# Optimization experiments

Hardware: AMD Instinct MI355X
Metric: run time of the kernel (lower is better)

Reference implementation:

```python
import jax, jax.numpy as jnp
import numpy as np

N_NODES = 100000
N_EDGES = 3200000
IN_CH = 256
HIDDEN = 64
OUT_CH = 128


def setup_inputs() -> dict:
    key = jax.random.key(0)
    ks = jax.random.split(key, 6)
    x = jax.random.normal(ks[0], (N_NODES, IN_CH), dtype=jnp.float32)
    edge_index = jax.random.randint(ks[1], (2, N_EDGES), 0, N_NODES, dtype=jnp.int64)
    W1 = jax.random.normal(ks[2], (IN_CH, HIDDEN), dtype=jnp.float32) * (1.0 / np.sqrt(IN_CH))
    b1 = jnp.zeros((HIDDEN,), dtype=jnp.float32)
    W2 = jax.random.normal(ks[3], (HIDDEN, OUT_CH), dtype=jnp.float32) * (1.0 / np.sqrt(HIDDEN))
    b2 = jnp.zeros((OUT_CH,), dtype=jnp.float32)
    fcW = jax.random.normal(ks[4], (2, OUT_CH), dtype=jnp.float32) * (1.0 / np.sqrt(OUT_CH))
    fcb = jnp.zeros((2,), dtype=jnp.float32)
    return {"x": x, "edge_index": edge_index, "W1": W1, "b1": b1,
            "W2": W2, "b2": b2, "fcW": fcW, "fcb": fcb}


def _gcn_conv(x, edge_index, W, b):
    """PyG GCNConv: linear transform, add self-loops, symmetric D^-1/2 A D^-1/2 aggregation, bias."""
    N = x.shape[0]
    h = x @ W  # [N, F_out]
    loops = jnp.arange(N, dtype=edge_index.dtype)
    row = jnp.concatenate([edge_index[0], loops])  # source nodes
    col = jnp.concatenate([edge_index[1], loops])  # destination nodes
    deg = jax.ops.segment_sum(jnp.ones_like(col, dtype=h.dtype), col, num_segments=N)
    dinv = jnp.where(deg > 0, jax.lax.rsqrt(deg), 0.0)
    norm = dinv[row] * dinv[col]  # [E+N]
    out = jax.ops.segment_sum(h[row] * norm[:, None], col, num_segments=N)
    return out + b


def reference(x, edge_index, W1, b1, W2, b2, fcW, fcb):
    h = jax.nn.relu(_gcn_conv(x, edge_index, W1, b1))
    h = jax.nn.relu(_gcn_conv(h, edge_index, W2, b2))
    g = jnp.mean(h, axis=0)  # [OUT_CH]
    return g @ fcW.T + fcb   # [2]
```

## Files before the change

kernel.cpp:

```cpp
#include <hip/hip_runtime.h>

#define N_NODES 100000
#define N_EDGES 3200000
#define C_IN 256
#define C_H 64
#define C_OUT 128
#define NB 391
#define G2F 625
#define NTILES 6250
#define CH1 8192

typedef unsigned int u32;
typedef unsigned short u16;
typedef unsigned long long u64;
typedef __attribute__((ext_vector_type(8))) short bf16x8;
typedef __attribute__((ext_vector_type(4))) float f32x4;

__device__ __forceinline__ float bflo(u32 p) {
    union { u32 i; float f; } v; v.i = p << 16; return v.f;
}
__device__ __forceinline__ float bfhi(u32 p) {
    union { u32 i; float f; } v; v.i = p & 0xffff0000u; return v.f;
}
__device__ __forceinline__ float bf2f(u16 u) {
    union { u32 i; float f; } v; v.i = ((u32)u) << 16; return v.f;
}
__device__ __forceinline__ u16 f2bf(float f) {
    union { float f; u32 i; } v; v.f = f;
    u32 x = v.i;
    return (u16)((x + 0x7fffu + ((x >> 16) & 1u)) >> 16);
}

__global__ void k_detect(const void* __restrict__ x, const void* __restrict__ ei,
                         const void* __restrict__ b1, const void* __restrict__ b2,
                         const void* __restrict__ fcW, const void* __restrict__ fcb,
                         int* __restrict__ flags,
                         float* __restrict__ b1c, float* __restrict__ b2c,
                         float* __restrict__ fcWc, float* __restrict__ fcbc) {
    __shared__ int sf[2];
    int t = threadIdx.x;
    if (t < 64) {
        u32 w = ((const u32*)x)[t];
        u32 low = w & 0xffffu;
        int e = (int)((low >> 7) & 0xff);
        bool inw = (e > 96 && e < 160) || (low == 0);
        u64 m = __ballot(inw);
        if (t == 0) sf[0] = (__popcll(m) >= 60) ? 1 : 0;
    } else if (t < 128) {
        int i = t - 64;
        u32 w = ((const u32*)ei)[2 * i + 1];
        u64 m = __ballot(w == 0);
        if (i == 0) sf[1] = (m == ~0ull) ? 1 : 0;
    }
    __syncthreads();
    if (t == 0) { flags[0] = sf[0]; flags[1] = sf[1]; }
    int isbf = sf[0];
    if (isbf) {
        const u16* p1 = (const u16*)b1;  const u16* p2 = (const u16*)b2;
        const u16* pw = (const u16*)fcW; const u16* pb = (const u16*)fcb;
        for (int i = t; i < C_H; i += 256) b1c[i] = bf2f(p1[i]);
        for (int i = t; i < C_OUT; i += 256) b2c[i] = bf2f(p2[i]);
        for (int i = t; i < 2 * C_OUT; i += 256) fcWc[i] = bf2f(pw[i]);
        for (int i = t; i < 2; i += 256) fcbc[i] = bf2f(pb[i]);
    } else {
        const float* p1 = (const float*)b1;  const float* p2 = (const float*)b2;
        const float* pw = (const float*)fcW; const float* pb = (const float*)fcb;
        for (int i = t; i < C_H; i += 256) b1c[i] = p1[i];
        for (int i = t; i < C_OUT; i += 256) b2c[i] = p2[i];
        for (int i = t; i < 2 * C_OUT; i += 256) fcWc[i] = pw[i];
        for (int i = t; i < 2; i += 256) fcbc[i] = pb[i];
    }
}

__global__ __launch_bounds__(256) void k_prep(const void* __restrict__ W1,
                                              const void* __restrict__ W2,
                                              const int* __restrict__ flags,
                                              u16* __restrict__ W1m, u16* __restrict__ W2m,
                                              u32* __restrict__ bucket_cnt) {
    int b = blockIdx.x, t = threadIdx.x;
    int isbf = flags[0];
    int i = b * 256 + t;
    if (i < NB) bucket_cnt[i] = 0;
    if (i < C_IN * C_H) {
        const u16* w1b = (const u16*)W1; const float* w1f = (const float*)W1;
        int j = i & 7, lane = (i >> 3) & 63, nt = (i >> 9) & 3, k0 = i >> 11;
        int k = k0 * 32 + ((lane >> 4) & 3) * 8 + j;
        int n = nt * 16 + (lane & 15);
        W1m[i] = isbf ? w1b[k * C_H + n] : f2bf(w1f[k * C_H + n]);
    } else {
        int i2 = i - C_IN * C_H;
        const u16* w2b = (const u16*)W2; const float* w2f = (const float*)W2;
        int j = i2 & 7, lane = (i2 >> 3) & 63, nt = (i2 >> 9) & 7, k0 = (i2 >> 12) & 1;
        int k = k0 * 32 + ((lane >> 4) & 3) * 8 + j;
        int n = nt * 16 + (lane & 15);
        W2m[i2] = isbf ? w2b[k * C_OUT + n] : f2bf(w2f[k * C_OUT + n]);
    }
}

__global__ __launch_bounds__(256) void k_hist1(const int* __restrict__ ei,
                                               const int* __restrict__ flags,
                                               u32* __restrict__ bucket_cnt) {
    __shared__ u32 h[NB];
    int t = threadIdx.x;
    int is64 = flags[1];
    for (int i = t; i < NB; i += 256) h[i] = 0;
    __syncthreads();
    int e0 = blockIdx.x * CH1;
    int nv = min(CH1, N_EDGES - e0);
    for (int i = t; i < nv; i += 256) {
        int e = e0 + i;
        int d = is64 ? ei[2 * (N_EDGES + e)] : ei[N_EDGES + e];
        atomicAdd(&h[d >> 8], 1u);
    }
    __syncthreads();
    for (int i = t; i < NB; i += 256)
        if (h[i]) atomicAdd(&bucket_cnt[i], h[i]);
}

__global__ __launch_bounds__(512) void k_bscan(const u32* __restrict__ bucket_cnt,
                                               u32* __restrict__ bucket_base,
                                               u32* __restrict__ bucket_cursor,
                                               int* __restrict__ rowptr) {
    __shared__ u32 sm[512];
    int t = threadIdx.x;
    u32 v = (t < NB) ? bucket_cnt[t] : 0;
    sm[t] = v;
    __syncthreads();
    for (int off = 1; off < 512; off <<= 1) {
        u32 a = (t >= off) ? sm[t - off] : 0;
        __syncthreads();
        sm[t] += a;
        __syncthreads();
    }
    if (t < NB) {
        u32 excl = sm[t] - v;
        bucket_base[t] = excl;
        bucket_cursor[t] = excl;
    }
    if (t == 0) {
        bucket_base[NB] = N_EDGES;
        rowptr[N_NODES] = N_EDGES;
    }
}

__global__ __launch_bounds__(512) void k_scatter1(const int* __restrict__ ei,
                                                  const int* __restrict__ flags,
                                                  u32* __restrict__ bucket_cursor,
                                                  u32* __restrict__ ebuf) {
    __shared__ u32 cnt[NB];
    __shared__ u32 lcur[NB];
    __shared__ u32 gbase[NB];
    __shared__ u32 lofs[512];
    __shared__ u32 stp[CH1];
    __shared__ u16 stb[CH1];
    int t = threadIdx.x;
    int is64 = flags[1];
    int e0 = blockIdx.x * CH1;
    int nv = min(CH1, N_EDGES - e0);
    for (int i = t; i < NB; i += 512) { cnt[i] = 0; lcur[i] = 0; }
    __syncthreads();
    for (int i = t; i < nv; i += 512) {
        int e = e0 + i;
        int d = is64 ? ei[2 * (N_EDGES + e)] : ei[N_EDGES + e];
        atomicAdd(&cnt[d >> 8], 1u);
    }
    __syncthreads();
    u32 v = (t < NB) ? cnt[t] : 0;
    lofs[t] = v;
    __syncthreads();
    for (int off = 1; off < 512; off <<= 1) {
        u32 a = (t >= off) ? lofs[t - off] : 0;
        __syncthreads();
        lofs[t] += a;
        __syncthreads();
    }
    u32 excl = lofs[t] - v;
    __syncthreads();
    lofs[t] = excl;
    __syncthreads();
    for (int i = t; i < nv; i += 512) {
        int e = e0 + i;
        int d, s;
        if (is64) { d = ei[2 * (N_EDGES + e)]; s = ei[2 * e]; }
        else      { d = ei[N_EDGES + e];       s = ei[e]; }
        int b = d >> 8;
        u32 slot = lofs[b] + atomicAdd(&lcur[b], 1u);
        stp[slot] = ((u32)(d & 255) << 20) | (u32)s;
        stb[slot] = (u16)b;
    }
    __syncthreads();
    for (int b = t; b < NB; b += 512) {
        u32 c = cnt[b];
        gbase[b] = c ? atomicAdd(&bucket_cursor[b], c) : 0;
    }
    __syncthreads();
    for (int s = t; s < nv; s += 512) {
        int b = stb[s];
        ebuf[gbase[b] + (s - lofs[b])] = stp[s];
    }
}

__global__ __launch_bounds__(256) void k_scatter2(const u32* __restrict__ bucket_base,
                                                  const u32* __restrict__ ebuf,
                                                  int* __restrict__ rowptr,
                                                  float* __restrict__ dinv,
                                                  int* __restrict__ csr) {
    __shared__ int cnt[256];
    __shared__ int pfx[256];
    __shared__ int lcur[256];
    int b = blockIdx.x, t = threadIdx.x;
    int ebeg = (int)bucket_base[b], eend = (int)bucket_base[b + 1];
    cnt[t] = 0;
    lcur[t] = 0;
    __syncthreads();
    for (int i = ebeg + t; i < eend; i += 256)
        atomicAdd(&cnt[(ebuf[i] >> 20) & 255], 1);
    __syncthreads();
    int v = cnt[t];
    pfx[t] = v;
    __syncthreads();
    for (int off = 1; off < 256; off <<= 1) {
        int a = (t >= off) ? pfx[t - off] : 0;
        __syncthreads();
        pfx[t] += a;
        __syncthreads();
    }
    int node = (b << 8) + t;
    if (node < N_NODES) {
        rowptr[node] = ebeg + (pfx[t] - v);
        dinv[node] = rsqrtf((float)(v + 1));
    }
    __syncthreads();
    for (int i = ebeg + t; i < eend; i += 256) {
        u32 p = ebuf[i];
        int dl = (p >> 20) & 255;
        int pos = ebeg + (pfx[dl] - cnt[dl]) + atomicAdd(&lcur[dl], 1);
        csr[pos] = (int)(p & 0x1FFFFu);
    }
}

__global__ __launch_bounds__(256) void k_gemm1(const void* __restrict__ xv,
                                               const u16* __restrict__ W1m,
                                               const float* __restrict__ dinv,
                                               u16* __restrict__ g1,
                                               const int* __restrict__ flags) {
    __shared__ u16 wlds[C_IN * C_H];
    int t = threadIdx.x;
    int isbf = flags[0];
    {
        const uint4* src = (const uint4*)W1m;
        uint4* dst = (uint4*)wlds;
#pragma unroll
        for (int it = 0; it < 8; ++it) dst[t + it * 256] = src[t + it * 256];
    }
    __syncthreads();
    int w = t >> 6, lane = t & 63;
    int quad = lane >> 4, mrow = lane & 15;
    int m0 = blockIdx.x * 128 + w * 32;
    if (m0 >= N_NODES) return;

    bf16x8 a[2][8];
    if (isbf) {
        const u16* xb = (const u16*)xv;
#pragma unroll
        for (int mt = 0; mt < 2; ++mt)
#pragma unroll
            for (int k0 = 0; k0 < 8; ++k0)
                a[mt][k0] = *(const bf16x8*)(xb + (size_t)(m0 + mt * 16 + mrow) * C_IN + k0 * 32 + quad * 8);
    } else {
        const float* xf = (const float*)xv;
#pragma unroll
        for (int mt = 0; mt < 2; ++mt)
#pragma unroll
            for (int k0 = 0; k0 < 8; ++k0) {
                const float* p = xf + (size_t)(m0 + mt * 16 + mrow) * C_IN + k0 * 32 + quad * 8;
                float4 v0 = *(const float4*)p;
                float4 v1 = *(const float4*)(p + 4);
                bf16x8 r;
                r[0] = (short)f2bf(v0.x); r[1] = (short)f2bf(v0.y);
                r[2] = (short)f2bf(v0.z); r[3] = (short)f2bf(v0.w);
                r[4] = (short)f2bf(v1.x); r[5] = (short)f2bf(v1.y);
                r[6] = (short)f2bf(v1.z); r[7] = (short)f2bf(v1.w);
                a[mt][k0] = r;
            }
    }

    float dv0[4], dv1[4];
#pragma unroll
    for (int r = 0; r < 4; ++r) {
        dv0[r] = dinv[m0 + quad * 4 + r];
        dv1[r] = dinv[m0 + 16 + quad * 4 + r];
    }

#pragma unroll
    for (int nt = 0; nt < 4; ++nt) {
        bf16x8 b[8];
#pragma unroll
        for (int k0 = 0; k0 < 8; ++k0)
            b[k0] = *(const bf16x8*)&wlds[((k0 * 4 + nt) * 64 + lane) * 8];
        f32x4 acc0 = {0.f, 0.f, 0.f, 0.f};
        f32x4 acc1 = {0.f, 0.f, 0.f, 0.f};
#pragma unroll
        for (int k0 = 0; k0 < 8; ++k0) {
            acc0 = __builtin_amdgcn_mfma_f32_16x16x32_bf16(a[0][k0], b[k0], acc0, 0, 0, 0);
            acc1 = __builtin_amdgcn_mfma_f32_16x16x32_bf16(a[1][k0], b[k0], acc1, 0, 0, 0);
        }
        int ch = nt * 16 + mrow;
#pragma unroll
        for (int r = 0; r < 4; ++r) {
            g1[(size_t)(m0 + quad * 4 + r) * C_H + ch] = f2bf(acc0[r] * dv0[r]);
            g1[(size_t)(m0 + 16 + quad * 4 + r) * C_H + ch] = f2bf(acc1[r] * dv1[r]);
        }
    }
}

template <int MODE>
__global__ __launch_bounds__(256) void k_gatherT(const int* __restrict__ rowptr,
                                                 const int* __restrict__ csr_src,
                                                 const float* __restrict__ dinv,
                                                 const u16* __restrict__ g,
                                                 const float* __restrict__ bias,
                                                 void* __restrict__ outv) {
    int t = threadIdx.x;
    int w = t >> 6, lane = t & 63;
    int half = lane >> 5, j = lane & 31;
    int n = blockIdx.x * 8 + w * 2 + half;
    int beg = rowptr[n], end = rowptr[n + 1];
    float sA = 0.f, sB = 0.f;
    int e = beg;
    for (; e + 7 < end; e += 8) {
        int s[8]; u32 p[8];
#pragma unroll
        for (int q = 0; q < 8; ++q) s[q] = csr_src[e + q];
#pragma unroll
        for (int q = 0; q < 8; ++q) p[q] = *(const u32*)(g + s[q] * C_H + 2 * j);
#pragma unroll
        for (int q = 0; q < 8; ++q) {
            sA += bflo(p[q]);
            sB += bfhi(p[q]);
        }
    }
    for (; e + 3 < end; e += 4) {
        int s[4]; u32 p[4];
#pragma unroll
        for (int q = 0; q < 4; ++q) s[q] = csr_src[e + q];
#pragma unroll
        for (int q = 0; q < 4; ++q) p[q] = *(const u32*)(g + s[q] * C_H + 2 * j);
#pragma unroll
        for (int q = 0; q < 4; ++q) {
            sA += bflo(p[q]);
            sB += bfhi(p[q]);
        }
    }
    for (; e < end; ++e) {
        int s0 = csr_src[e];
        u32 p0 = *(const u32*)(g + s0 * C_H + 2 * j);
        sA += bflo(p0);
        sB += bfhi(p0);
    }
    float dn = dinv[n];
    u32 gn = *(const u32*)(g + n * C_H + 2 * j);
    float vA = dn * (sA + bflo(gn));
    float vB = dn * (sB + bfhi(gn));
    if (MODE == 0) {
        float aA = fmaxf(vA + bias[2 * j], 0.f);
        float aB = fmaxf(vB + bias[2 * j + 1], 0.f);
        u32 pk = (u32)f2bf(dn * aA) | ((u32)f2bf(dn * aB) << 16);
        ((u32*)outv)[n * 32 + j] = pk;
    } else {
        ((float2*)outv)[n * 32 + j] = make_float2(vA, vB);
    }
}

__global__ __launch_bounds__(256) void k_fused2(const float* __restrict__ agg,
                                                const u16* __restrict__ W2m,
                                                const float* __restrict__ b2c,
                                                float* __restrict__ partial) {
    __shared__ float psum[4 * 8 * 64];
    int t = threadIdx.x;
    int w = t >> 6, lane = t & 63;
    int quad = lane >> 4, m = lane & 15;

    bf16x8 b[2][8];
#pragma unroll
    for (int k0 = 0; k0 < 2; ++k0)
#pragma unroll
        for (int nt = 0; nt < 8; ++nt)
            b[k0][nt] = *(const bf16x8*)&W2m[((k0 * 8 + nt) * 64 + lane) * 8];

    float pacc[8] = {0.f, 0.f, 0.f, 0.f, 0.f, 0.f, 0.f, 0.f};
    float bias[8];
#pragma unroll
    for (int nt = 0; nt < 8; ++nt) bias[nt] = b2c[nt * 16 + m];

    for (int tile = blockIdx.x * 4 + w; tile < NTILES; tile += G2F * 4) {
        const float* arow = agg + (size_t)(tile * 16 + m) * C_H + quad * 8;
        bf16x8 a[2];
#pragma unroll
        for (int k0 = 0; k0 < 2; ++k0) {
            float4 v0 = *(const float4*)(arow + k0 * 32);
            float4 v1 = *(const float4*)(arow + k0 * 32 + 4);
            bf16x8 r;
            r[0] = (short)f2bf(v0.x); r[1] = (short)f2bf(v0.y);
            r[2] = (short)f2bf(v0.z); r[3] = (short)f2bf(v0.w);
            r[4] = (short)f2bf(v1.x); r[5] = (short)f2bf(v1.y);
            r[6] = (short)f2bf(v1.z); r[7] = (short)f2bf(v1.w);
            a[k0] = r;
        }
#pragma unroll
        for (int nt = 0; nt < 8; ++nt) {
            f32x4 acc = {0.f, 0.f, 0.f, 0.f};
            acc = __builtin_amdgcn_mfma_f32_16x16x32_bf16(a[0], b[0][nt], acc, 0, 0, 0);
            acc = __builtin_amdgcn_mfma_f32_16x16x32_bf16(a[1], b[1][nt], acc, 0, 0, 0);
#pragma unroll
            for (int r = 0; r < 4; ++r)
                pacc[nt] += fmaxf(acc[r] + bias[nt], 0.f);
        }
    }
#pragma unroll
    for (int nt = 0; nt < 8; ++nt) psum[(w * 8 + nt) * 64 + lane] = pacc[nt];
    __syncthreads();
    if (t < 128) {
        int nt = t >> 4, m2 = t & 15;
        float s = 0.f;
#pragma unroll
        for (int ww = 0; ww < 4; ++ww)
#pragma unroll
            for (int q = 0; q < 4; ++q)
                s += psum[(ww * 8 + nt) * 64 + q * 16 + m2];
        partial[blockIdx.x * C_OUT + t] = s;
    }
}

__global__ __launch_bounds__(512) void k_final(const float* __restrict__ partial,
                                               const float* __restrict__ fcWc,
                                               const float* __restrict__ fcbc,
                                               void* __restrict__ out,
                                               const int* __restrict__ flags) {
    __shared__ float sm[512];
    __shared__ float red[256];
    int t = threadIdx.x;
    int f = t & 127, c = t >> 7;
    float s = 0.f;
    for (int b = c; b < G2F; b += 4) s += partial[b * 128 + f];
    sm[t] = s;
    __syncthreads();
    if (t < 128) {
        float gm = (sm[t] + sm[t + 128] + sm[t + 256] + sm[t + 384]) * (1.0f / (float)N_NODES);
        red[t] = gm * fcWc[t];
        red[128 + t] = gm * fcWc[128 + t];
    }
    __syncthreads();
    for (int off = 64; off >= 1; off >>= 1) {
        if (t < off) {
            red[t] += red[t + off];
            red[128 + t] += red[128 + t + off];
        }
        __syncthreads();
    }
    if (t == 0) {
        float o0 = red[0] + fcbc[0];
        float o1 = red[128] + fcbc[1];
        if (flags[0]) {
            u16* ob = (u16*)out;
            ob[0] = f2bf(o0);
            ob[1] = f2bf(o1);
        } else {
            float* of = (float*)out;
            of[0] = o0;
            of[1] = o1;
        }
    }
}

#define OFF_FLAGS   0u
#define OFF_DINV    512u
#define OFF_ROWPTR  400896u
#define OFF_BCNT    801280u
#define OFF_BBASE   802944u
#define OFF_BCUR    804608u
#define OFF_CSR     1201664u
#define OFF_H1      14001664u
#define OFF_A1      26801664u
#define OFF_AGG     39601664u
#define OFF_PART    65201664u
#define OFF_W1C     65728000u
#define OFF_W2C     65760768u
#define OFF_B1C     65777152u
#define OFF_B2C     65777408u
#define OFF_FCWC    65777920u
#define OFF_FCBC    65778944u

extern "C" void kernel_launch(void* const* d_in, const int* in_sizes, int n_in,
                              void* d_out, int out_size, void* d_ws, size_t ws_size,
                              hipStream_t stream) {
    (void)in_sizes; (void)n_in; (void)out_size; (void)ws_size;
    const void* x   = d_in[0];
    const int*  ei  = (const int*)d_in[1];
    const void* W1  = d_in[2];
    const void* b1  = d_in[3];
    const void* W2  = d_in[4];
    const void* b2  = d_in[5];
    const void* fcW = d_in[6];
    const void* fcb = d_in[7];

    char* ws = (char*)d_ws;
    int*   flags  = (int*)(ws + OFF_FLAGS);
    float* dinv   = (float*)(ws + OFF_DINV);
    int*   rowptr = (int*)(ws + OFF_ROWPTR);
    u32*   bcnt   = (u32*)(ws + OFF_BCNT);
    u32*   bbase  = (u32*)(ws + OFF_BBASE);
    u32*   bcur   = (u32*)(ws + OFF_BCUR);
    int*   csr    = (int*)(ws + OFF_CSR);
    u16*   g1     = (u16*)(ws + OFF_H1);
    u16*   a1s    = (u16*)(ws + OFF_A1);
    float* agg    = (float*)(ws + OFF_AGG);
    u32*   ebuf   = (u32*)(ws + OFF_AGG);
    float* partial= (float*)(ws + OFF_PART);
    u16*   W1m    = (u16*)(ws + OFF_W1C);
    u16*   W2m    = (u16*)(ws + OFF_W2C);
    float* b1c    = (float*)(ws + OFF_B1C);
    float* b2c    = (float*)(ws + OFF_B2C);
    float* fcWc   = (float*)(ws + OFF_FCWC);
    float* fcbc   = (float*)(ws + OFF_FCBC);

    k_detect<<<1, 256, 0, stream>>>(x, ei, b1, b2, fcW, fcb,
                                    flags, b1c, b2c, fcWc, fcbc);
    k_prep<<<96, 256, 0, stream>>>(W1, W2, flags, W1m, W2m, bcnt);
    k_hist1<<<NB, 256, 0, stream>>>(ei, flags, bcnt);
    k_bscan<<<1, 512, 0, stream>>>(bcnt, bbase, bcur, rowptr);
    k_scatter1<<<NB, 512, 0, stream>>>(ei, flags, bcur, ebuf);
    k_scatter2<<<NB, 256, 0, stream>>>(bbase, ebuf, rowptr, dinv, csr);
    k_gemm1<<<(N_NODES + 127) / 128, 256, 0, stream>>>(x, W1m, dinv, g1, flags);
    k_gatherT<0><<<N_NODES / 8, 256, 0, stream>>>(rowptr, csr, dinv, g1, b1c, (void*)a1s);
    k_gatherT<1><<<N_NODES / 8, 256, 0, stream>>>(rowptr, csr, dinv, a1s, (const float*)nullptr, (void*)agg);
    k_fused2<<<G2F, 256, 0, stream>>>(agg, W2m, b2c, partial);
    k_final<<<1, 512, 0, stream>>>(partial, fcWc, fcbc, (void*)d_out, flags);
}
```

Measured before the change: 419.0 us.

## Restructure gather to one wave per node with 16-byte loads, store bf16 aggregate

```diff
diff --git a/kernel.cpp b/kernel.cpp
--- a/kernel.cpp
+++ b/kernel.cpp
@@ -320,59 +320,68 @@
                                                  const float* __restrict__ dinv,
                                                  const u16* __restrict__ g,
                                                  const float* __restrict__ bias,
-                                                 void* __restrict__ outv) {
+                                                 u16* __restrict__ out) {
     int t = threadIdx.x;
     int w = t >> 6, lane = t & 63;
-    int half = lane >> 5, j = lane & 31;
-    int n = blockIdx.x * 8 + w * 2 + half;
+    int grp = lane >> 3, c = lane & 7;
+    int n = blockIdx.x * 4 + w;
     int beg = rowptr[n], end = rowptr[n + 1];
-    float sA = 0.f, sB = 0.f;
-    int e = beg;
-    for (; e + 7 < end; e += 8) {
-        int s[8]; u32 p[8];
-#pragma unroll
-        for (int q = 0; q < 8; ++q) s[q] = csr_src[e + q];
-#pragma unroll
-        for (int q = 0; q < 8; ++q) p[q] = *(const u32*)(g + s[q] * C_H + 2 * j);
-#pragma unroll
-        for (int q = 0; q < 8; ++q) {
-            sA += bflo(p[q]);
-            sB += bfhi(p[q]);
+    float acc[8] = {0.f, 0.f, 0.f, 0.f, 0.f, 0.f, 0.f, 0.f};
+    int e = beg + grp;
+    for (; e + 8 < end; e += 16) {
+        int sa = csr_src[e];
+        int sb = csr_src[e + 8];
+        uint4 pa = *(const uint4*)(g + (size_t)sa * C_H + c * 8);
+        uint4 pb = *(const uint4*)(g + (size_t)sb * C_H + c * 8);
+        acc[0] += bflo(pa.x); acc[1] += bfhi(pa.x);
+        acc[2] += bflo(pa.y); acc[3] += bfhi(pa.y);
+        acc[4] += bflo(pa.z); acc[5] += bfhi(pa.z);
+        acc[6] += bflo(pa.w); acc[7] += bfhi(pa.w);
+        acc[0] += bflo(pb.x); acc[1] += bfhi(pb.x);
+        acc[2] += bflo(pb.y); acc[3] += bfhi(pb.y);
+        acc[4] += bflo(pb.z); acc[5] += bfhi(pb.z);
+        acc[6] += bflo(pb.w); acc[7] += bfhi(pb.w);
+    }
+    if (e < end) {
+        int sa = csr_src[e];
+        uint4 pa = *(const uint4*)(g + (size_t)sa * C_H + c * 8);
+        acc[0] += bflo(pa.x); acc[1] += bfhi(pa.x);
+        acc[2] += bflo(pa.y); acc[3] += bfhi(pa.y);
+        acc[4] += bflo(pa.z); acc[5] += bfhi(pa.z);
+        acc[6] += bflo(pa.w); acc[7] += bfhi(pa.w);
+    }
+#pragma unroll
+    for (int i = 0; i < 8; ++i) {
+        acc[i] += __shfl_xor(acc[i], 8, 64);
+        acc[i] += __shfl_xor(acc[i], 16, 64);
+        acc[i] += __shfl_xor(acc[i], 32, 64);
+    }
+    if (grp == 0) {
+        float dn = dinv[n];
+        uint4 pn = *(const uint4*)(g + (size_t)n * C_H + c * 8);
+        float sf[8];
+        sf[0] = bflo(pn.x); sf[1] = bfhi(pn.x);
+        sf[2] = bflo(pn.y); sf[3] = bfhi(pn.y);
+        sf[4] = bflo(pn.z); sf[5] = bfhi(pn.z);
+        sf[6] = bflo(pn.w); sf[7] = bfhi(pn.w);
+        u32 res[4];
+#pragma unroll
+        for (int k = 0; k < 4; ++k) {
+            float vA = dn * (acc[2 * k] + sf[2 * k]);
+            float vB = dn * (acc[2 * k + 1] + sf[2 * k + 1]);
+            if (MODE == 0) {
+                vA = dn * fmaxf(vA + bias[c * 8 + 2 * k], 0.f);
+                vB = dn * fmaxf(vB + bias[c * 8 + 2 * k + 1], 0.f);
+            }
+            res[k] = (u32)f2bf(vA) | ((u32)f2bf(vB) << 16);
         }
-    }
-    for (; e + 3 < end; e += 4) {
-        int s[4]; u32 p[4];
-#pragma unroll
-        for (int q = 0; q < 4; ++q) s[q] = csr_src[e + q];
-#pragma unroll
-        for (int q = 0; q < 4; ++q) p[q] = *(const u32*)(g + s[q] * C_H + 2 * j);
-#pragma unroll
-        for (int q = 0; q < 4; ++q) {
-            sA += bflo(p[q]);
-            sB += bfhi(p[q]);
-        }
-    }
-    for (; e < end; ++e) {
-        int s0 = csr_src[e];
-        u32 p0 = *(const u32*)(g + s0 * C_H + 2 * j);
-        sA += bflo(p0);
-        sB += bfhi(p0);
-    }
-    float dn = dinv[n];
-    u32 gn = *(const u32*)(g + n * C_H + 2 * j);
-    float vA = dn * (sA + bflo(gn));
-    float vB = dn * (sB + bfhi(gn));
-    if (MODE == 0) {
-        float aA = fmaxf(vA + bias[2 * j], 0.f);
-        float aB = fmaxf(vB + bias[2 * j + 1], 0.f);
-        u32 pk = (u32)f2bf(dn * aA) | ((u32)f2bf(dn * aB) << 16);
-        ((u32*)outv)[n * 32 + j] = pk;
-    } else {
-        ((float2*)outv)[n * 32 + j] = make_float2(vA, vB);
-    }
-}
-
-__global__ __launch_bounds__(256) void k_fused2(const float* __restrict__ agg,
+        uint4 pk;
+        pk.x = res[0]; pk.y = res[1]; pk.z = res[2]; pk.w = res[3];
+        *(uint4*)(out + (size_t)n * C_H + c * 8) = pk;
+    }
+}
+
+__global__ __launch_bounds__(256) void k_fused2(const u16* __restrict__ aggb,
                                                 const u16* __restrict__ W2m,
                                                 const float* __restrict__ b2c,
                                                 float* __restrict__ partial) {
@@ -394,24 +403,14 @@
     for (int nt = 0; nt < 8; ++nt) bias[nt] = b2c[nt * 16 + m];
 
     for (int tile = blockIdx.x * 4 + w; tile < NTILES; tile += G2F * 4) {
-        const float* arow = agg + (size_t)(tile * 16 + m) * C_H + quad * 8;
-        bf16x8 a[2];
-#pragma unroll
-        for (int k0 = 0; k0 < 2; ++k0) {
-            float4 v0 = *(const float4*)(arow + k0 * 32);
-            float4 v1 = *(const float4*)(arow + k0 * 32 + 4);
-            bf16x8 r;
-            r[0] = (short)f2bf(v0.x); r[1] = (short)f2bf(v0.y);
-            r[2] = (short)f2bf(v0.z); r[3] = (short)f2bf(v0.w);
-            r[4] = (short)f2bf(v1.x); r[5] = (short)f2bf(v1.y);
-            r[6] = (short)f2bf(v1.z); r[7] = (short)f2bf(v1.w);
-            a[k0] = r;
-        }
+        const u16* arow = aggb + (size_t)(tile * 16 + m) * C_H + quad * 8;
+        bf16x8 a0 = *(const bf16x8*)(arow);
+        bf16x8 a1 = *(const bf16x8*)(arow + 32);
 #pragma unroll
         for (int nt = 0; nt < 8; ++nt) {
             f32x4 acc = {0.f, 0.f, 0.f, 0.f};
-            acc = __builtin_amdgcn_mfma_f32_16x16x32_bf16(a[0], b[0][nt], acc, 0, 0, 0);
-            acc = __builtin_amdgcn_mfma_f32_16x16x32_bf16(a[1], b[1][nt], acc, 0, 0, 0);
+            acc = __builtin_amdgcn_mfma_f32_16x16x32_bf16(a0, b[0][nt], acc, 0, 0, 0);
+            acc = __builtin_amdgcn_mfma_f32_16x16x32_bf16(a1, b[1][nt], acc, 0, 0, 0);
 #pragma unroll
             for (int r = 0; r < 4; ++r)
                 pacc[nt] += fmaxf(acc[r] + bias[nt], 0.f);
@@ -514,7 +513,7 @@
     int*   csr    = (int*)(ws + OFF_CSR);
     u16*   g1     = (u16*)(ws + OFF_H1);
     u16*   a1s    = (u16*)(ws + OFF_A1);
-    float* agg    = (float*)(ws + OFF_AGG);
+    u16*   aggb   = (u16*)(ws + OFF_AGG);
     u32*   ebuf   = (u32*)(ws + OFF_AGG);
     float* partial= (float*)(ws + OFF_PART);
     u16*   W1m    = (u16*)(ws + OFF_W1C);
@@ -532,8 +531,8 @@
     k_scatter1<<<NB, 512, 0, stream>>>(ei, flags, bcur, ebuf);
     k_scatter2<<<NB, 256, 0, stream>>>(bbase, ebuf, rowptr, dinv, csr);
     k_gemm1<<<(N_NODES + 127) / 128, 256, 0, stream>>>(x, W1m, dinv, g1, flags);
-    k_gatherT<0><<<N_NODES / 8, 256, 0, stream>>>(rowptr, csr, dinv, g1, b1c, (void*)a1s);
-    k_gatherT<1><<<N_NODES / 8, 256, 0, stream>>>(rowptr, csr, dinv, a1s, (const float*)nullptr, (void*)agg);
-    k_fused2<<<G2F, 256, 0, stream>>>(agg, W2m, b2c, partial);
+    k_gatherT<0><<<N_NODES / 4, 256, 0, stream>>>(rowptr, csr, dinv, g1, b1c, a1s);
+    k_gatherT<1><<<N_NODES / 4, 256, 0, stream>>>(rowptr, csr, dinv, a1s, (const float*)nullptr, aggb);
+    k_fused2<<<G2F, 256, 0, stream>>>(aggb, W2m, b2c, partial);
     k_final<<<1, 512, 0, stream>>>(partial, fcWc, fcbc, (void*)d_out, flags);
 }
```

Result: no change. 415.8 us (-0.8%).
